# Optimization experiments

Hardware: AMD Instinct MI355X
Metric: run time of the kernel (lower is better)

## Reference

```python
import jax, jax.numpy as jnp
import numpy as np
import math

B, T, C, H, S_CACHE = 2, 1024, 2048, 16, 1024
DK = C // H


def setup_inputs() -> dict:
    key = jax.random.key(0)
    ks = jax.random.split(key, 7)
    x = jax.random.normal(ks[0], (B, T, C), dtype=jnp.float32)
    cache_k = jax.random.normal(ks[1], (B, H, S_CACHE, DK), dtype=jnp.float32)
    cache_v = jax.random.normal(ks[2], (B, H, S_CACHE, DK), dtype=jnp.float32)
    scale = 0.02
    Wq = jax.random.normal(ks[3], (C, C), dtype=jnp.float32) * scale
    Wk = jax.random.normal(ks[4], (C, C), dtype=jnp.float32) * scale
    Wv = jax.random.normal(ks[5], (C, C), dtype=jnp.float32) * scale
    Wo = jax.random.normal(ks[6], (C, C), dtype=jnp.float32) * scale
    return {"x": x, "cache_k": cache_k, "cache_v": cache_v,
            "Wq": Wq, "Wk": Wk, "Wv": Wv, "Wo": Wo}


def reference(x, cache_k, cache_v, Wq, Wk, Wv, Wo):
    b, t, c = x.shape
    h = cache_k.shape[1]
    dk = c // h
    # nn.Linear: y = x @ W.T  (weights stored [out, in])
    Q = (x @ Wq.T).reshape(b, t, h, dk).transpose(0, 2, 1, 3)  # [B,H,T,dk]
    K = (x @ Wk.T).reshape(b, t, h, dk).transpose(0, 2, 1, 3)
    V = (x @ Wv.T).reshape(b, t, h, dk).transpose(0, 2, 1, 3)
    K = jnp.concatenate([cache_k, K], axis=2)  # [B,H,S,dk]
    V = jnp.concatenate([cache_v, V], axis=2)
    s = K.shape[2]
    scores = jnp.einsum('bhtd,bhsd->bhts', Q, K) / math.sqrt(dk)
    # faithful to the source: mask = tril(ones(T, S)) (no cache offset); T==1 -> all ones
    if t == 1:
        mask = jnp.ones((1, s), dtype=jnp.float32)
    else:
        mask = jnp.tril(jnp.ones((t, s), dtype=jnp.float32))
    scores = jnp.where(mask == 0, jnp.float32(-jnp.inf), scores)
    attn = jax.nn.softmax(scores, axis=-1)
    out = jnp.einsum('bhts,bhsd->bhtd', attn, V)
    out = out.transpose(0, 2, 1, 3).reshape(b, t, c)
    return (out @ Wo.T, K, V)
```

## Files before the change

kernel.cpp:

```cpp
#include <hip/hip_runtime.h>

typedef unsigned short u16;
typedef short bf16x8 __attribute__((ext_vector_type(8)));
typedef float f32x4 __attribute__((ext_vector_type(4)));
typedef unsigned short u16x4 __attribute__((ext_vector_type(4)));

#define AS1 __attribute__((address_space(1)))
#define AS3 __attribute__((address_space(3)))

__device__ __forceinline__ u16 f2bf(float f) {
    unsigned u = __float_as_uint(f);
    u += 0x7fff + ((u >> 16) & 1);
    return (u16)(u >> 16);
}

__device__ __forceinline__ void gld16(const void* g, void* l) {
    __builtin_amdgcn_global_load_lds((const AS1 void*)g, (AS3 void*)l, 16, 0, 0);
}

__global__ void convall_kernel(const float* __restrict__ x,  const float* __restrict__ wq,
                               const float* __restrict__ wk, const float* __restrict__ wv,
                               const float* __restrict__ wo,
                               u16* __restrict__ xb, u16* __restrict__ wqkv, u16* __restrict__ wob) {
    int t = blockIdx.x * 256 + threadIdx.x;
    const float* srcs[5] = { x, wq, wk, wv, wo };
    u16* dsts[5] = { xb, wqkv, wqkv + 4194304, wqkv + 8388608, wob };
#pragma unroll
    for (int r = 0; r < 5; r++) {
        f32x4 v = ((const f32x4*)srcs[r])[t];
        u16x4 o = { f2bf(v.x), f2bf(v.y), f2bf(v.z), f2bf(v.w) };
        ((u16x4*)dsts[r])[t] = o;
    }
}

__global__ void cachek_kernel(const float* __restrict__ ck, float* __restrict__ kout,
                              u16* __restrict__ kcb) {
    const int n4 = (2 * 16 * 1024 * 128) / 4;
    int i = blockIdx.x * 256 + threadIdx.x;
    int stride = gridDim.x * 256;
    for (; i < n4; i += stride) {
        f32x4 v = ((const f32x4*)ck)[i];
        int bh = i >> 15;
        ((f32x4*)kout)[i + bh * 32768] = v;
        u16x4 o = { f2bf(v.x), f2bf(v.y), f2bf(v.z), f2bf(v.w) };
        ((u16x4*)kcb)[i] = o;
    }
}

__global__ void vtrans_kernel(const float* __restrict__ cv, float* __restrict__ vout,
                              u16* __restrict__ vtb) {
    __shared__ u16 tile[64 * 65];
    const int bh = blockIdx.x;
    const int s0 = blockIdx.y * 64;
    const int d0 = blockIdx.z * 64;
    const float* src = cv + (size_t)bh * 1024 * 128;
#pragma unroll
    for (int i = 0; i < 16; i++) {
        int e = i * 256 + threadIdx.x;
        int sr = e >> 6, dc = e & 63;
        float v = src[(size_t)(s0 + sr) * 128 + d0 + dc];
        vout[((size_t)bh * 2048 + s0 + sr) * 128 + d0 + dc] = v;
        tile[sr * 65 + dc] = f2bf(v);
    }
    __syncthreads();
    u16* dst = vtb + (size_t)bh * 128 * 1024;
#pragma unroll
    for (int i = 0; i < 16; i++) {
        int e = i * 256 + threadIdx.x;
        int dr = e >> 6, sc = e & 63;
        dst[(size_t)(d0 + dr) * 1024 + s0 + sc] = tile[sc * 65 + dr];
    }
}

#define PH_COMPUTE(MO, NO, NN, BREG) \
    __builtin_amdgcn_s_barrier(); \
    asm volatile("s_waitcnt lgkmcnt(0)" ::: "memory"); \
    __builtin_amdgcn_sched_barrier(0); \
    __builtin_amdgcn_s_setprio(1); \
    _Pragma("unroll") \
    for (int mf = 0; mf < 4; mf++) { \
        _Pragma("unroll") \
        for (int nf = 0; nf < NN; nf++) { \
            _Pragma("unroll") \
            for (int kk = 0; kk < 2; kk++) \
                acc[MO + mf][NO + nf] = __builtin_amdgcn_mfma_f32_16x16x32_bf16( \
                    aF[mf][kk], BREG[nf][kk], acc[MO + mf][NO + nf], 0, 0, 0); \
        } \
    } \
    __builtin_amdgcn_s_setprio(0); \
    __builtin_amdgcn_s_barrier();

#define HALF(P, S1, S2, S3, VM) \
    { \
        _Pragma("unroll") \
        for (int mf = 0; mf < 4; mf++) \
            _Pragma("unroll") \
            for (int kk = 0; kk < 2; kk++) aF[mf][kk] = rdA(P, mf, kk); \
        _Pragma("unroll") \
        for (int nf = 0; nf < 2; nf++) \
            _Pragma("unroll") \
            for (int kk = 0; kk < 2; kk++) b01[nf][kk] = rdB(P, nf, kk); \
        S1; \
        PH_COMPUTE(0, 0, 2, b01) \
        _Pragma("unroll") \
        for (int kk = 0; kk < 2; kk++) b2[0][kk] = rdB(P, 2, kk); \
        S2; \
        PH_COMPUTE(0, 2, 1, b2) \
        _Pragma("unroll") \
        for (int mf = 0; mf < 4; mf++) \
            _Pragma("unroll") \
            for (int kk = 0; kk < 2; kk++) aF[mf][kk] = rdA(P, 4 + mf, kk); \
        S3; \
        PH_COMPUTE(4, 2, 1, b2) \
        VM; \
        PH_COMPUTE(4, 0, 2, b01) \
    }

__global__ __launch_bounds__(512, 2) void gemm_qkv_kernel(
    const u16* __restrict__ A, const u16* __restrict__ Bm,
    u16* __restrict__ qout, float* __restrict__ kout, float* __restrict__ vout) {
    __shared__ u16 Ab[2][16384];
    __shared__ u16 Bb[2][12288];
    const int tid = threadIdx.x;
    const int lane = tid & 63, wv8 = tid >> 6;
    const int wrow = (wv8 >> 2) * 128;
    const int wcol = (wv8 & 3) * 48;
    const int m0 = blockIdx.y * 256, n0 = blockIdx.x * 192;
    const int frow = lane & 15, fq = lane >> 4;
    const int swz = frow & 7;

    f32x4 acc[8][3];
#pragma unroll
    for (int a = 0; a < 8; a++)
#pragma unroll
        for (int b = 0; b < 3; b++) acc[a][b] = (f32x4){0.f, 0.f, 0.f, 0.f};

    auto stA = [&](int kt, int half) {
        u16* dst = &Ab[kt & 1][half * 8192];
#pragma unroll
        for (int j = 0; j < 2; j++) {
            int L = j * 512 + tid;
            int row = L >> 3, c = (L & 7) ^ (row & 7);
            gld16(A + (size_t)(m0 + half * 128 + row) * 2048 + kt * 64 + c * 8,
                  dst + j * 4096 + wv8 * 512);
        }
    };
    auto stB = [&](int kt, int ch) {
        u16* dst = &Bb[kt & 1][ch * 4096];
        int row = tid >> 3, c = (tid & 7) ^ (row & 7);
        gld16(Bm + (size_t)(n0 + ch * 64 + row) * 2048 + kt * 64 + c * 8,
              dst + wv8 * 512);
    };
    auto rdA = [&](int p, int mf, int kk) {
        int r = wrow + mf * 16 + frow;
        return *(const bf16x8*)(&Ab[p][r * 64 + (((kk << 2) + fq) ^ swz) * 8]);
    };
    auto rdB = [&](int p, int nf, int kk) {
        int r = wcol + nf * 16 + frow;
        return *(const bf16x8*)(&Bb[p][r * 64 + (((kk << 2) + fq) ^ swz) * 8]);
    };

    bf16x8 aF[4][2], b01[2][2], b2[1][2];

    stA(0, 0); stA(0, 1); stB(0, 0); stB(0, 1); stB(0, 2);
    stB(1, 0); stB(1, 1); stB(1, 2);
    asm volatile("s_waitcnt vmcnt(3)" ::: "memory");
    __builtin_amdgcn_s_barrier();

    for (int u = 0; u < 30; u += 2) {
        HALF(0, stA(u + 1, 0), stA(u + 1, 1),
             (stB(u + 2, 0), stB(u + 2, 1), stB(u + 2, 2)),
             asm volatile("s_waitcnt vmcnt(3)" ::: "memory"))
        HALF(1, stA(u + 2, 0), stA(u + 2, 1),
             (stB(u + 3, 0), stB(u + 3, 1), stB(u + 3, 2)),
             asm volatile("s_waitcnt vmcnt(3)" ::: "memory"))
    }
    HALF(0, stA(31, 0), stA(31, 1), (void)0,
         asm volatile("s_waitcnt vmcnt(0)" ::: "memory"))
    HALF(1, (void)0, (void)0, (void)0, (void)0)

#pragma unroll
    for (int fm = 0; fm < 8; fm++) {
#pragma unroll
        for (int fn = 0; fn < 3; fn++) {
#pragma unroll
            for (int r = 0; r < 4; r++) {
                int m = m0 + wrow + fm * 16 + fq * 4 + r;
                int n = n0 + wcol + fn * 16 + frow;
                float v = acc[fm][fn][r];
                int b = m >> 10, t = m & 1023;
                int sect = n >> 11, nn = n & 2047;
                int h = nn >> 7, d = nn & 127;
                size_t bh = (size_t)(b * 16 + h);
                if (sect == 0)
                    qout[(bh * 1024 + t) * 128 + d] = f2bf(v * 0.08838834764831843f);
                else if (sect == 1)
                    kout[(bh * 2048 + 1024 + t) * 128 + d] = v;
                else
                    vout[(bh * 2048 + 1024 + t) * 128 + d] = v;
            }
        }
    }
}

__global__ __launch_bounds__(256) void gemm_out_kernel(
    const u16* __restrict__ A, const u16* __restrict__ Bm, float* __restrict__ cout) {
    __shared__ u16 As[64 * 64];
    __shared__ u16 Bs[128 * 64];
    const int tid = threadIdx.x;
    const int lane = tid & 63, wv = tid >> 6;
    const int wn = wv * 32;
    const int m0 = blockIdx.y * 64, n0 = blockIdx.x * 128;
    const int frow = lane & 15, fq = lane >> 4;
    const int swz = frow & 7;

    f32x4 acc[4][2];
#pragma unroll
    for (int a = 0; a < 4; a++)
#pragma unroll
        for (int b = 0; b < 2; b++) acc[a][b] = (f32x4){0.f, 0.f, 0.f, 0.f};

    for (int k0 = 0; k0 < 2048; k0 += 64) {
        __syncthreads();
#pragma unroll
        for (int i = 0; i < 2; i++) {
            int L = i * 256 + tid;
            int row = L >> 3;
            int c = (L & 7) ^ (row & 7);
            gld16(A + (size_t)(m0 + row) * 2048 + k0 + c * 8, As + i * 2048 + wv * 512);
        }
#pragma unroll
        for (int i = 0; i < 4; i++) {
            int L = i * 256 + tid;
            int row = L >> 3;
            int c = (L & 7) ^ (row & 7);
            gld16(Bm + (size_t)(n0 + row) * 2048 + k0 + c * 8, Bs + i * 2048 + wv * 512);
        }
        __syncthreads();
#pragma unroll
        for (int kk = 0; kk < 2; kk++) {
            bf16x8 aF[4], bF[2];
#pragma unroll
            for (int f = 0; f < 4; f++)
                aF[f] = *(const bf16x8*)(As + (f * 16 + frow) * 64 + ((kk * 4 + fq) ^ swz) * 8);
#pragma unroll
            for (int f = 0; f < 2; f++)
                bF[f] = *(const bf16x8*)(Bs + (wn + f * 16 + frow) * 64 + ((kk * 4 + fq) ^ swz) * 8);
#pragma unroll
            for (int fm = 0; fm < 4; fm++)
#pragma unroll
                for (int fn = 0; fn < 2; fn++)
                    acc[fm][fn] = __builtin_amdgcn_mfma_f32_16x16x32_bf16(aF[fm], bF[fn], acc[fm][fn], 0, 0, 0);
        }
    }

#pragma unroll
    for (int fm = 0; fm < 4; fm++) {
#pragma unroll
        for (int fn = 0; fn < 2; fn++) {
#pragma unroll
            for (int r = 0; r < 4; r++) {
                int m = m0 + fm * 16 + fq * 4 + r;
                int n = n0 + wn + fn * 16 + frow;
                cout[(size_t)m * 2048 + n] = acc[fm][fn][r];
            }
        }
    }
}

__global__ __launch_bounds__(256) void attn_kernel(
    const u16* __restrict__ Qb, const u16* __restrict__ Kcb,
    const u16* __restrict__ Vtb, u16* __restrict__ AOb,
    float* __restrict__ PO, float* __restrict__ PML) {
    __shared__ u16 Qs[64 * 128];
    __shared__ u16 Ks[64 * 128];
    __shared__ u16 Vs[128 * 64];
    __shared__ u16 Ps[64 * 64];
    const int bid = blockIdx.x;
    int bh, qi, st_begin, st_end, cidx;
    bool partial;
    if (bid < 512) {
        qi = 15 - (bid >> 6);
        int j = bid & 63;
        bh = j >> 1;
        int c = j & 1;
        int n = qi + 1, h0 = (n + 1) >> 1;
        st_begin = c ? h0 : 0;
        st_end = c ? n : h0;
        partial = true;
        cidx = c * 256 + bh * 8 + (qi - 8);
    } else {
        int j = bid - 512;
        qi = 7 - (j >> 5);
        bh = j & 31;
        st_begin = 0; st_end = qi + 1;
        partial = false; cidx = 0;
    }
    const int t0 = qi * 64;
    const int tid = threadIdx.x, lane = tid & 63, wv = tid >> 6;
    const int row_w = wv * 16;
    const int frow = lane & 15, fq = lane >> 4;
    const int swz = frow & 7;

    const u16* Qg = Qb + ((size_t)bh * 1024 + t0) * 128;
#pragma unroll
    for (int i = 0; i < 4; i++) {
        int L = i * 256 + tid;
        int row = L >> 4;
        int c = (L & 15) ^ (row & 7);
        gld16(Qg + row * 128 + c * 8, Qs + i * 2048 + wv * 512);
    }

    float mrow[4], lrow[4];
    f32x4 Oacc[8];
#pragma unroll
    for (int r = 0; r < 4; r++) { mrow[r] = -1e30f; lrow[r] = 0.f; }
#pragma unroll
    for (int fd = 0; fd < 8; fd++) Oacc[fd] = (f32x4){0.f, 0.f, 0.f, 0.f};

    for (int st = st_begin; st < st_end; st++) {
        int s0 = st * 64;
        __syncthreads();
        const u16* Kg = Kcb + ((size_t)bh * 1024 + s0) * 128;
#pragma unroll
        for (int i = 0; i < 4; i++) {
            int L = i * 256 + tid;
            int row = L >> 4;
            int c = (L & 15) ^ (row & 7);
            gld16(Kg + row * 128 + c * 8, Ks + i * 2048 + wv * 512);
        }
        const u16* Vg = Vtb + (size_t)bh * 131072 + s0;
#pragma unroll
        for (int i = 0; i < 4; i++) {
            int L = i * 256 + tid;
            int row = L >> 3;
            int c = (L & 7) ^ (row & 7);
            gld16(Vg + row * 1024 + c * 8, Vs + i * 2048 + wv * 512);
        }
        __syncthreads();

        f32x4 S[4];
#pragma unroll
        for (int fn = 0; fn < 4; fn++) S[fn] = (f32x4){0.f, 0.f, 0.f, 0.f};
#pragma unroll
        for (int kk = 0; kk < 4; kk++) {
            bf16x8 aF = *(const bf16x8*)(Qs + (row_w + frow) * 128 + ((kk * 4 + fq) ^ swz) * 8);
#pragma unroll
            for (int fn = 0; fn < 4; fn++) {
                bf16x8 bF = *(const bf16x8*)(Ks + (fn * 16 + frow) * 128 + ((kk * 4 + fq) ^ swz) * 8);
                S[fn] = __builtin_amdgcn_mfma_f32_16x16x32_bf16(aF, bF, S[fn], 0, 0, 0);
            }
        }

        if (st == qi) {
#pragma unroll
            for (int fn = 0; fn < 4; fn++)
#pragma unroll
                for (int r = 0; r < 4; r++) {
                    int t = t0 + row_w + fq * 4 + r;
                    int s = s0 + fn * 16 + frow;
                    if (s > t) S[fn][r] = -1e30f;
                }
        }

#pragma unroll
        for (int r = 0; r < 4; r++) {
            float mx = fmaxf(fmaxf(S[0][r], S[1][r]), fmaxf(S[2][r], S[3][r]));
            mx = fmaxf(mx, __shfl_xor(mx, 1));
            mx = fmaxf(mx, __shfl_xor(mx, 2));
            mx = fmaxf(mx, __shfl_xor(mx, 4));
            mx = fmaxf(mx, __shfl_xor(mx, 8));
            float mnew = fmaxf(mrow[r], mx);
            float alpha = __expf(mrow[r] - mnew);
            float rs = 0.f;
#pragma unroll
            for (int fn = 0; fn < 4; fn++) {
                float p = __expf(S[fn][r] - mnew);
                S[fn][r] = p;
                rs += p;
            }
            rs += __shfl_xor(rs, 1);
            rs += __shfl_xor(rs, 2);
            rs += __shfl_xor(rs, 4);
            rs += __shfl_xor(rs, 8);
            mrow[r] = mnew;
            lrow[r] = lrow[r] * alpha + rs;
#pragma unroll
            for (int fd = 0; fd < 8; fd++) Oacc[fd][r] *= alpha;
        }

#pragma unroll
        for (int fn = 0; fn < 4; fn++)
#pragma unroll
            for (int r = 0; r < 4; r++) {
                int pr = row_w + fq * 4 + r;
                int c = fn * 2 + (frow >> 3);
                Ps[pr * 64 + ((c ^ (pr & 7)) * 8) + (frow & 7)] = f2bf(S[fn][r]);
            }

#pragma unroll
        for (int ks = 0; ks < 2; ks++) {
            int rr = row_w + frow;
            bf16x8 aP = *(const bf16x8*)(Ps + rr * 64 + ((ks * 4 + fq) ^ (rr & 7)) * 8);
#pragma unroll
            for (int fd = 0; fd < 8; fd++) {
                int vr = fd * 16 + frow;
                bf16x8 bV = *(const bf16x8*)(Vs + vr * 64 + ((ks * 4 + fq) ^ (vr & 7)) * 8);
                Oacc[fd] = __builtin_amdgcn_mfma_f32_16x16x32_bf16(aP, bV, Oacc[fd], 0, 0, 0);
            }
        }
    }

    if (partial) {
        float* Od = PO + (size_t)cidx * 8192;
#pragma unroll
        for (int r = 0; r < 4; r++) {
            int row = row_w + fq * 4 + r;
#pragma unroll
            for (int fd = 0; fd < 8; fd++)
                Od[row * 128 + fd * 16 + frow] = Oacc[fd][r];
        }
        if (frow == 0) {
#pragma unroll
            for (int r = 0; r < 4; r++) {
                int row = row_w + fq * 4 + r;
                PML[cidx * 128 + row * 2] = mrow[r];
                PML[cidx * 128 + row * 2 + 1] = lrow[r];
            }
        }
    } else {
        const int b = bh >> 4, h = bh & 15;
#pragma unroll
        for (int r = 0; r < 4; r++) {
            float rl = 1.0f / lrow[r];
            int t = t0 + row_w + fq * 4 + r;
#pragma unroll
            for (int fd = 0; fd < 8; fd++) {
                int col = h * 128 + fd * 16 + frow;
                AOb[((size_t)b * 1024 + t) * 2048 + col] = f2bf(Oacc[fd][r] * rl);
            }
        }
    }
}

__global__ __launch_bounds__(256) void attn_merge_kernel(
    const float* __restrict__ PO, const float* __restrict__ PML, u16* __restrict__ AOb) {
    const int idx = blockIdx.x;
    const int bh = idx >> 3, qi = 8 + (idx & 7);
    const int t0 = qi * 64;
    const int b = bh >> 4, h = bh & 15;
    const int tid = threadIdx.x;
    const int row = tid >> 2, cg = tid & 3;
    const float* O0 = PO + (size_t)idx * 8192;
    const float* O1 = PO + (size_t)(256 + idx) * 8192;
    float m0 = PML[idx * 128 + row * 2],        l0 = PML[idx * 128 + row * 2 + 1];
    float m1 = PML[(256 + idx) * 128 + row * 2], l1 = PML[(256 + idx) * 128 + row * 2 + 1];
    float mm = fmaxf(m0, m1);
    float w0 = __expf(m0 - mm), w1 = __expf(m1 - mm);
    float inv = 1.0f / (l0 * w0 + l1 * w1);
    u16* dst = AOb + ((size_t)b * 1024 + t0 + row) * 2048 + h * 128 + cg * 32;
#pragma unroll
    for (int j = 0; j < 8; j++) {
        f32x4 a = *(const f32x4*)(O0 + row * 128 + cg * 32 + j * 4);
        f32x4 c = *(const f32x4*)(O1 + row * 128 + cg * 32 + j * 4);
        u16x4 o = { f2bf((a.x * w0 + c.x * w1) * inv), f2bf((a.y * w0 + c.y * w1) * inv),
                    f2bf((a.z * w0 + c.z * w1) * inv), f2bf((a.w * w0 + c.w * w1) * inv) };
        *(u16x4*)(dst + j * 4) = o;
    }
}

extern "C" void kernel_launch(void* const* d_in, const int* in_sizes, int n_in,
                              void* d_out, int out_size, void* d_ws, size_t ws_size,
                              hipStream_t stream) {
    const float* x  = (const float*)d_in[0];
    const float* ck = (const float*)d_in[1];
    const float* cv = (const float*)d_in[2];
    const float* Wq = (const float*)d_in[3];
    const float* Wk = (const float*)d_in[4];
    const float* Wv = (const float*)d_in[5];
    const float* Wo = (const float*)d_in[6];

    float* out  = (float*)d_out;
    float* Kout = out + 4194304;
    float* Vout = out + 12582912;

    u16* xb   = (u16*)d_ws;
    u16* Wqkv = xb + 4194304;
    u16* Wob  = Wqkv + 12582912;
    u16* Qb   = Wob + 4194304;
    u16* Kcb  = Qb + 4194304;
    u16* Vtb  = Kcb + 4194304;
    u16* AOb  = Vtb + 4194304;
    float* PO  = (float*)Wqkv;
    float* PML = PO + 4194304;

    convall_kernel<<<4096, 256, 0, stream>>>(x, Wq, Wk, Wv, Wo, xb, Wqkv, Wob);
    cachek_kernel<<<1024, 256, 0, stream>>>(ck, Kout, Kcb);
    vtrans_kernel<<<dim3(32, 16, 2), 256, 0, stream>>>(cv, Vout, Vtb);

    gemm_qkv_kernel<<<dim3(32, 8), 512, 0, stream>>>(xb, Wqkv, Qb, Kout, Vout);
    attn_kernel<<<768, 256, 0, stream>>>(Qb, Kcb, Vtb, AOb, PO, PML);
    attn_merge_kernel<<<256, 256, 0, stream>>>(PO, PML, AOb);
    gemm_out_kernel<<<dim3(16, 32), 256, 0, stream>>>(AOb, Wob, out);
}
```

Measured before the change: 315.7 us.

## Reshape QKV GEMM wave tiles to 64x96 and triple-buffer the B tile

The QKV projection GEMM's per-wave tile changes from 128x48 (2x4 wave grid) to 64x96 (4x2 wave grid). This changes the LDS fragment-read mix per k-step from 8 A plus 3 B to 4 A plus 6 B fragments. The B shared-memory buffer becomes triple-buffered with a 6-iteration unrolled rotation, so prefetches no longer overwrite the buffer being read, and a partial lgkmcnt wait is added before the first MFMA phase. In exchange, LDS use rises by one extra B buffer, which may pressure the two-blocks-per-CU occupancy target, and the schedule is more intricate.

```diff
diff --git a/kernel.cpp b/kernel.cpp
--- a/kernel.cpp
+++ b/kernel.cpp
@@ -72,7 +72,7 @@
     }
 }
 
-#define PH_COMPUTE(MO, NO, NN, BREG) \
+#define PH16(NF0) \
     __builtin_amdgcn_s_barrier(); \
     asm volatile("s_waitcnt lgkmcnt(0)" ::: "memory"); \
     __builtin_amdgcn_sched_barrier(0); \
@@ -80,63 +80,66 @@
     _Pragma("unroll") \
     for (int mf = 0; mf < 4; mf++) { \
         _Pragma("unroll") \
-        for (int nf = 0; nf < NN; nf++) { \
+        for (int nq = 0; nq < 2; nq++) { \
             _Pragma("unroll") \
             for (int kk = 0; kk < 2; kk++) \
-                acc[MO + mf][NO + nf] = __builtin_amdgcn_mfma_f32_16x16x32_bf16( \
-                    aF[mf][kk], BREG[nf][kk], acc[MO + mf][NO + nf], 0, 0, 0); \
+                acc[mf][NF0 + nq] = __builtin_amdgcn_mfma_f32_16x16x32_bf16( \
+                    aF[mf][kk], bF[nq][kk], acc[mf][NF0 + nq], 0, 0, 0); \
         } \
     } \
     __builtin_amdgcn_s_setprio(0); \
     __builtin_amdgcn_s_barrier();
 
-#define HALF(P, S1, S2, S3, VM) \
-    { \
+#define ITER(PA, PB, S1, S2, S3, VM) { \
+    _Pragma("unroll") \
+    for (int mf = 0; mf < 4; mf++) \
         _Pragma("unroll") \
-        for (int mf = 0; mf < 4; mf++) \
-            _Pragma("unroll") \
-            for (int kk = 0; kk < 2; kk++) aF[mf][kk] = rdA(P, mf, kk); \
+        for (int kk = 0; kk < 2; kk++) aF[mf][kk] = rdA(PA, mf, kk); \
+    _Pragma("unroll") \
+    for (int nq = 0; nq < 2; nq++) \
         _Pragma("unroll") \
-        for (int nf = 0; nf < 2; nf++) \
-            _Pragma("unroll") \
-            for (int kk = 0; kk < 2; kk++) b01[nf][kk] = rdB(P, nf, kk); \
-        S1; \
-        PH_COMPUTE(0, 0, 2, b01) \
+        for (int kk = 0; kk < 2; kk++) bF[nq][kk] = rdB(PB, nq, kk); \
+    S1; \
+    asm volatile("s_waitcnt lgkmcnt(8)" ::: "memory"); \
+    PH16(0) \
+    _Pragma("unroll") \
+    for (int nq = 0; nq < 2; nq++) \
         _Pragma("unroll") \
-        for (int kk = 0; kk < 2; kk++) b2[0][kk] = rdB(P, 2, kk); \
-        S2; \
-        PH_COMPUTE(0, 2, 1, b2) \
+        for (int kk = 0; kk < 2; kk++) bF[nq][kk] = rdB(PB, 2 + nq, kk); \
+    S2; \
+    PH16(2) \
+    _Pragma("unroll") \
+    for (int nq = 0; nq < 2; nq++) \
         _Pragma("unroll") \
-        for (int mf = 0; mf < 4; mf++) \
-            _Pragma("unroll") \
-            for (int kk = 0; kk < 2; kk++) aF[mf][kk] = rdA(P, 4 + mf, kk); \
-        S3; \
-        PH_COMPUTE(4, 2, 1, b2) \
-        VM; \
-        PH_COMPUTE(4, 0, 2, b01) \
-    }
+        for (int kk = 0; kk < 2; kk++) bF[nq][kk] = rdB(PB, 4 + nq, kk); \
+    S3; \
+    VM; \
+    PH16(4) \
+}
+
+#define VM3 asm volatile("s_waitcnt vmcnt(3)" ::: "memory")
 
 __global__ __launch_bounds__(512, 2) void gemm_qkv_kernel(
     const u16* __restrict__ A, const u16* __restrict__ Bm,
     u16* __restrict__ qout, float* __restrict__ kout, float* __restrict__ vout) {
     __shared__ u16 Ab[2][16384];
-    __shared__ u16 Bb[2][12288];
+    __shared__ u16 Bb[3][12288];
     const int tid = threadIdx.x;
     const int lane = tid & 63, wv8 = tid >> 6;
-    const int wrow = (wv8 >> 2) * 128;
-    const int wcol = (wv8 & 3) * 48;
+    const int wrow = (wv8 >> 1) * 64;
+    const int wcol = (wv8 & 1) * 96;
     const int m0 = blockIdx.y * 256, n0 = blockIdx.x * 192;
     const int frow = lane & 15, fq = lane >> 4;
     const int swz = frow & 7;
 
-    f32x4 acc[8][3];
-#pragma unroll
-    for (int a = 0; a < 8; a++)
-#pragma unroll
-        for (int b = 0; b < 3; b++) acc[a][b] = (f32x4){0.f, 0.f, 0.f, 0.f};
-
-    auto stA = [&](int kt, int half) {
-        u16* dst = &Ab[kt & 1][half * 8192];
+    f32x4 acc[4][6];
+#pragma unroll
+    for (int a = 0; a < 4; a++)
+#pragma unroll
+        for (int b = 0; b < 6; b++) acc[a][b] = (f32x4){0.f, 0.f, 0.f, 0.f};
+
+    auto stA = [&](int buf, int kt, int half) {
+        u16* dst = &Ab[buf][half * 8192];
 #pragma unroll
         for (int j = 0; j < 2; j++) {
             int L = j * 512 + tid;
@@ -145,8 +148,8 @@
                   dst + j * 4096 + wv8 * 512);
         }
     };
-    auto stB = [&](int kt, int ch) {
-        u16* dst = &Bb[kt & 1][ch * 4096];
+    auto stB = [&](int buf, int kt, int ch) {
+        u16* dst = &Bb[buf][ch * 4096];
         int row = tid >> 3, c = (tid & 7) ^ (row & 7);
         gld16(Bm + (size_t)(n0 + ch * 64 + row) * 2048 + kt * 64 + c * 8,
               dst + wv8 * 512);
@@ -160,29 +163,36 @@
         return *(const bf16x8*)(&Bb[p][r * 64 + (((kk << 2) + fq) ^ swz) * 8]);
     };
 
-    bf16x8 aF[4][2], b01[2][2], b2[1][2];
-
-    stA(0, 0); stA(0, 1); stB(0, 0); stB(0, 1); stB(0, 2);
-    stB(1, 0); stB(1, 1); stB(1, 2);
-    asm volatile("s_waitcnt vmcnt(3)" ::: "memory");
+    bf16x8 aF[4][2], bF[2][2];
+
+    stA(0, 0, 0); stA(0, 0, 1);
+    stB(0, 0, 0); stB(0, 0, 1); stB(0, 0, 2);
+    stB(1, 1, 0); stB(1, 1, 1); stB(1, 1, 2);
+    VM3;
     __builtin_amdgcn_s_barrier();
 
-    for (int u = 0; u < 30; u += 2) {
-        HALF(0, stA(u + 1, 0), stA(u + 1, 1),
-             (stB(u + 2, 0), stB(u + 2, 1), stB(u + 2, 2)),
-             asm volatile("s_waitcnt vmcnt(3)" ::: "memory"))
-        HALF(1, stA(u + 2, 0), stA(u + 2, 1),
-             (stB(u + 3, 0), stB(u + 3, 1), stB(u + 3, 2)),
-             asm volatile("s_waitcnt vmcnt(3)" ::: "memory"))
-    }
-    HALF(0, stA(31, 0), stA(31, 1), (void)0,
+    for (int u = 0; u < 30; u += 6) {
+        ITER(0, 0, stA(1, u + 1, 0), stA(1, u + 1, 1),
+             (stB(2, u + 2, 0), stB(2, u + 2, 1), stB(2, u + 2, 2)), VM3)
+        ITER(1, 1, stA(0, u + 2, 0), stA(0, u + 2, 1),
+             (stB(0, u + 3, 0), stB(0, u + 3, 1), stB(0, u + 3, 2)), VM3)
+        ITER(0, 2, stA(1, u + 3, 0), stA(1, u + 3, 1),
+             (stB(1, u + 4, 0), stB(1, u + 4, 1), stB(1, u + 4, 2)), VM3)
+        ITER(1, 0, stA(0, u + 4, 0), stA(0, u + 4, 1),
+             (stB(2, u + 5, 0), stB(2, u + 5, 1), stB(2, u + 5, 2)), VM3)
+        ITER(0, 1, stA(1, u + 5, 0), stA(1, u + 5, 1),
+             (stB(0, u + 6, 0), stB(0, u + 6, 1), stB(0, u + 6, 2)), VM3)
+        ITER(1, 2, stA(0, u + 6, 0), stA(0, u + 6, 1),
+             (stB(1, u + 7, 0), stB(1, u + 7, 1), stB(1, u + 7, 2)), VM3)
+    }
+    ITER(0, 0, stA(1, 31, 0), stA(1, 31, 1), (void)0,
          asm volatile("s_waitcnt vmcnt(0)" ::: "memory"))
-    HALF(1, (void)0, (void)0, (void)0, (void)0)
-
-#pragma unroll
-    for (int fm = 0; fm < 8; fm++) {
-#pragma unroll
-        for (int fn = 0; fn < 3; fn++) {
+    ITER(1, 1, (void)0, (void)0, (void)0, (void)0)
+
+#pragma unroll
+    for (int fm = 0; fm < 4; fm++) {
+#pragma unroll
+        for (int fn = 0; fn < 6; fn++) {
 #pragma unroll
             for (int r = 0; r < 4; r++) {
                 int m = m0 + wrow + fm * 16 + fq * 4 + r;
```

Result: no change. 312.8 us (-0.9%).
